# Kernel optimization log

Measured on AMD Instinct MI355X. Metric: run time of the kernel, lower is better.

The kernel has to match this reference:

```python
import jax, jax.numpy as jnp
import numpy as np

# Module hyperparams (from init_kwargs)
VX, VY = 0.16, 0.16
PC_RANGE = (0.0, -39.68, -3.0, 69.12, 39.68, 1.0)
X_OFFSET = VX / 2 + PC_RANGE[0]
Y_OFFSET = VY / 2 + PC_RANGE[1]
X_L = int((PC_RANGE[3] - PC_RANGE[0]) / VX)  # 432
Y_L = int((PC_RANGE[4] - PC_RANGE[1]) / VY)  # 496
IN_CH, OUT_CH = 9, 64
BN_EPS = 1e-3
P, N_MAX, B = 40000, 32, 4


def setup_inputs() -> dict:
    key = jax.random.key(0)
    k1, k2, k3 = jax.random.split(key, 3)
    pillars = jax.random.normal(k1, (P, N_MAX, 4), dtype=jnp.float32)
    # Unique (per batch) pillar coordinates so the scatter is well-defined.
    rng = np.random.default_rng(0)
    per = P // B
    rows = []
    for b in range(B):
        lin = rng.choice(Y_L * X_L, size=per, replace=False)
        ys, xs = lin // X_L, lin % X_L
        rows.append(np.stack([np.full(per, b, np.int32), xs.astype(np.int32), ys.astype(np.int32)], axis=1))
    coors_batch = jnp.asarray(np.concatenate(rows, axis=0))  # (P,3): [b, x, y]
    npoints_per_pillar = jax.random.randint(k2, (P,), 1, N_MAX + 1, dtype=jnp.int32)
    # Learned params: 1x1 Conv1d weight (no bias) + BN affine
    W = jax.random.normal(k3, (OUT_CH, IN_CH), dtype=jnp.float32) * 0.1
    gamma = jnp.ones((OUT_CH,), dtype=jnp.float32)
    beta = jnp.zeros((OUT_CH,), dtype=jnp.float32)
    return {"pillars": pillars, "coors_batch": coors_batch,
            "npoints_per_pillar": npoints_per_pillar,
            "W": W, "gamma": gamma, "beta": beta, "batch_size": B}


def reference(pillars, coors_batch, npoints_per_pillar, W, gamma, beta, batch_size):
    npts = npoints_per_pillar.astype(pillars.dtype)
    # offset of each point from pillar mean (xyz)
    center = jnp.sum(pillars[:, :, :3], axis=1, keepdims=True) / npts[:, None, None]
    offset_pt_center = pillars[:, :, :3] - center                      # (P,N,3)
    cx = coors_batch[:, None, 1:2].astype(pillars.dtype) * VX + X_OFFSET
    cy = coors_batch[:, None, 2:3].astype(pillars.dtype) * VY + Y_OFFSET
    x_off = pillars[:, :, :1] - cx                                     # (P,N,1)
    y_off = pillars[:, :, 1:2] - cy                                    # (P,N,1)
    features = jnp.concatenate([pillars, offset_pt_center, x_off, y_off], axis=-1)  # (P,N,9)
    mask = (jnp.arange(N_MAX)[None, :] < npoints_per_pillar[:, None]).astype(features.dtype)
    features = features * mask[:, :, None]
    # 1x1 Conv1d == per-point channel mix -> (P, C_out, N)
    x = jnp.einsum('pnc,oc->pon', features, W)
    # BatchNorm1d (training-mode stats over pillar and point dims, biased var)
    mean = jnp.mean(x, axis=(0, 2))
    var = jnp.var(x, axis=(0, 2))
    x = gamma[None, :, None] * (x - mean[None, :, None]) * jax.lax.rsqrt(var[None, :, None] + BN_EPS) + beta[None, :, None]
    x = jax.nn.relu(x)
    pooled = jnp.max(x, axis=-1)                                       # (P, C_out)
    # Single vectorized scatter into BEV canvas: (B, Y, X, C) then -> (B, C, Y, X)
    canvas = jnp.zeros((batch_size, Y_L, X_L, OUT_CH), dtype=jnp.float32)
    canvas = canvas.at[coors_batch[:, 0], coors_batch[:, 2], coors_batch[:, 1]].set(pooled)
    return jnp.transpose(canvas, (0, 3, 1, 2))
```

## Files before the change

### kernel.cpp

```cpp
#include <hip/hip_runtime.h>
#include <math.h>

#define P_TOT 40000
#define NMAX 32
#define BATCH 4
#define YL 496
#define XL 432
#define CIN 9
#define COUT 64
#define NTRI 45
#define PN_F 1280000.0f

#define MAP_ELEMS (BATCH * YL * XL)
#define MAP_BYTES (MAP_ELEMS * 4)
#define STATS_OFF MAP_BYTES
#define POOLED_OFF (STATS_OFF + 256)

#define STATS_BLOCKS 512


__global__ __launch_bounds__(256) void k_stats(const float4* __restrict__ pillars,
                                               const int* __restrict__ coors,
                                               const int* __restrict__ npp,
                                               int* __restrict__ map,
                                               float* __restrict__ stats) {
    const int wave = threadIdx.x >> 6;
    const int lane = threadIdx.x & 63;
    const int half = lane >> 5;
    const int n = lane & 31;
    const int gw = blockIdx.x * 4 + wave;
    const int totalWaves = STATS_BLOCKS * 4;

    float s1[CIN];
    float s2[NTRI];
#pragma unroll
    for (int i = 0; i < CIN; i++) s1[i] = 0.0f;
#pragma unroll
    for (int i = 0; i < NTRI; i++) s2[i] = 0.0f;

    for (int p0 = gw * 2; p0 < P_TOT; p0 += totalWaves * 2) {
        int p = p0 + half;
        float4 q = pillars[(size_t)p * NMAX + n];

        float sx = q.x, sy = q.y, sz = q.z;
#pragma unroll
        for (int off = 1; off < 32; off <<= 1) {
            sx += __shfl_xor(sx, off, 32);
            sy += __shfl_xor(sy, off, 32);
            sz += __shfl_xor(sz, off, 32);
        }
        int npts = npp[p];
        float fn = (float)npts;
        float mx = sx / fn, my = sy / fn, mz = sz / fn;

        int xi = coors[p * 3 + 1];
        int yi = coors[p * 3 + 2];
        if (n == 0) {
            int b = coors[p * 3 + 0];
            map[(b * YL + yi) * XL + xi] = p;
        }
        float cx = (float)xi * 0.16f + 0.08f;
        float cy = (float)yi * 0.16f + (-39.6f);

        float msk = (n < npts) ? 1.0f : 0.0f;
        float f[CIN];
        f[0] = q.x * msk; f[1] = q.y * msk; f[2] = q.z * msk; f[3] = q.w * msk;
        f[4] = (q.x - mx) * msk; f[5] = (q.y - my) * msk; f[6] = (q.z - mz) * msk;
        f[7] = (q.x - cx) * msk; f[8] = (q.y - cy) * msk;

        int k = 0;
#pragma unroll
        for (int a = 0; a < CIN; a++) {
            s1[a] += f[a];
#pragma unroll
            for (int c = a; c < CIN; c++) s2[k++] += f[a] * f[c];
        }
    }

#pragma unroll
    for (int i = 0; i < CIN; i++) {
        float v = s1[i];
        for (int off = 1; off < 64; off <<= 1) v += __shfl_xor(v, off, 64);
        s1[i] = v;
    }
#pragma unroll
    for (int i = 0; i < NTRI; i++) {
        float v = s2[i];
        for (int off = 1; off < 64; off <<= 1) v += __shfl_xor(v, off, 64);
        s2[i] = v;
    }

    __shared__ float red[4][54];
    if (lane == 0) {
#pragma unroll
        for (int i = 0; i < CIN; i++) red[wave][i] = s1[i];
#pragma unroll
        for (int i = 0; i < NTRI; i++) red[wave][CIN + i] = s2[i];
    }
    __syncthreads();
    if (threadIdx.x < 54) {
        float v = red[0][threadIdx.x] + red[1][threadIdx.x] +
                  red[2][threadIdx.x] + red[3][threadIdx.x];
        atomicAdd(&stats[threadIdx.x], v);
    }
}

__global__ __launch_bounds__(256) void k_pool(const float4* __restrict__ pillars,
                                              const int* __restrict__ coors,
                                              const int* __restrict__ npp,
                                              const float* __restrict__ W,
                                              float* __restrict__ pooled) {
    int w = threadIdx.x >> 6;
    int lane = threadIdx.x & 63;
    int p = blockIdx.x * 4 + w;
    int n = lane & 31;

    float4 q = pillars[(size_t)p * NMAX + n];
    float sx = q.x, sy = q.y, sz = q.z;
#pragma unroll
    for (int off = 1; off < 32; off <<= 1) {
        sx += __shfl_xor(sx, off, 32);
        sy += __shfl_xor(sy, off, 32);
        sz += __shfl_xor(sz, off, 32);
    }
    int npts = __builtin_amdgcn_readfirstlane(npp[p]);
    float fn = (float)npts;
    float mx = sx / fn, my = sy / fn, mz = sz / fn;
    int xi = coors[p * 3 + 1];
    int yi = coors[p * 3 + 2];
    float cx = (float)xi * 0.16f + 0.08f;
    float cy = (float)yi * 0.16f + (-39.6f);

    const float* wr = W + lane * CIN;
    float w0 = wr[0], w1 = wr[1], w2 = wr[2], w3 = wr[3];
    float w4 = wr[4], w5 = wr[5], w6 = wr[6], w7 = wr[7], w8 = wr[8];
    float A0 = w0 + w4 + w7;
    float A1 = w1 + w5 + w8;
    float A2 = w2 + w6;
    float B = -(w4 * mx + w5 * my + w6 * mz + w7 * cx + w8 * cy);

    float m = (npts < NMAX) ? 0.0f : -INFINITY;
    for (int j = 0; j < npts; ++j) {
        float qx = __uint_as_float(__builtin_amdgcn_readlane(__float_as_uint(q.x), j));
        float qy = __uint_as_float(__builtin_amdgcn_readlane(__float_as_uint(q.y), j));
        float qz = __uint_as_float(__builtin_amdgcn_readlane(__float_as_uint(q.z), j));
        float qw = __uint_as_float(__builtin_amdgcn_readlane(__float_as_uint(q.w), j));
        float d = fmaf(A0, qx, fmaf(A1, qy, fmaf(A2, qz, fmaf(w3, qw, B))));
        m = fmaxf(m, d);
    }
    pooled[(size_t)p * COUT + lane] = m;
}

__global__ __launch_bounds__(256) void k_scatter(const int* __restrict__ map,
                                                 const float* __restrict__ pooled,
                                                 const float* __restrict__ W,
                                                 const float* __restrict__ gamma,
                                                 const float* __restrict__ beta,
                                                 const float* __restrict__ stats,
                                                 float* __restrict__ out) {
    __shared__ float ssc[COUT];
    __shared__ float ssh[COUT];
    if (threadIdx.x < COUT) {
        int o = threadIdx.x;
        float wv[CIN];
#pragma unroll
        for (int c = 0; c < CIN; c++) wv[c] = W[o * CIN + c];

        const float invPN = 1.0f / PN_F;
        float mu = 0.0f;
#pragma unroll
        for (int c = 0; c < CIN; c++) mu += wv[c] * (stats[c] * invPN);

        float ex2 = 0.0f;
        int k = 0;
#pragma unroll
        for (int a = 0; a < CIN; a++) {
#pragma unroll
            for (int c = a; c < CIN; c++) {
                float Mv = stats[CIN + k] * invPN;
                float t = wv[a] * wv[c] * Mv;
                ex2 += (a == c) ? t : 2.0f * t;
                k++;
            }
        }
        float var = ex2 - mu * mu;
        float sc = gamma[o] * rsqrtf(var + 1e-3f);
        ssc[o] = sc;
        ssh[o] = beta[o] - mu * sc;
    }
    __syncthreads();

    int i = blockIdx.x * 256 + threadIdx.x;
    if (i >= BATCH * YL * (XL / 4)) return;
    int x4 = i % (XL / 4);
    int r = i / (XL / 4);
    int y = r % YL;
    int b = r / YL;

    const int4 pid = *(const int4*)(map + (size_t)(b * YL + y) * XL + x4 * 4);
    size_t obase = ((size_t)(b * COUT) * YL + y) * XL + (size_t)x4 * 4;
    const size_t cstride = (size_t)YL * XL;

    const float4 ninf = make_float4(-INFINITY, -INFINITY, -INFINITY, -INFINITY);
#pragma unroll 4
    for (int c4 = 0; c4 < COUT / 4; c4++) {
        float4 r0 = ninf, r1 = ninf, r2 = ninf, r3 = ninf;
        if (pid.x >= 0) r0 = *(const float4*)(pooled + (size_t)pid.x * COUT + c4 * 4);
        if (pid.y >= 0) r1 = *(const float4*)(pooled + (size_t)pid.y * COUT + c4 * 4);
        if (pid.z >= 0) r2 = *(const float4*)(pooled + (size_t)pid.z * COUT + c4 * 4);
        if (pid.w >= 0) r3 = *(const float4*)(pooled + (size_t)pid.w * COUT + c4 * 4);
        float sc0 = ssc[c4 * 4 + 0], sh0 = ssh[c4 * 4 + 0];
        float sc1 = ssc[c4 * 4 + 1], sh1 = ssh[c4 * 4 + 1];
        float sc2 = ssc[c4 * 4 + 2], sh2 = ssh[c4 * 4 + 2];
        float sc3 = ssc[c4 * 4 + 3], sh3 = ssh[c4 * 4 + 3];
        float* o0 = out + obase + (size_t)(c4 * 4) * cstride;
        *(float4*)(o0) = make_float4(
            fmaxf(fmaf(sc0, r0.x, sh0), 0.f), fmaxf(fmaf(sc0, r1.x, sh0), 0.f),
            fmaxf(fmaf(sc0, r2.x, sh0), 0.f), fmaxf(fmaf(sc0, r3.x, sh0), 0.f));
        *(float4*)(o0 + cstride) = make_float4(
            fmaxf(fmaf(sc1, r0.y, sh1), 0.f), fmaxf(fmaf(sc1, r1.y, sh1), 0.f),
            fmaxf(fmaf(sc1, r2.y, sh1), 0.f), fmaxf(fmaf(sc1, r3.y, sh1), 0.f));
        *(float4*)(o0 + 2 * cstride) = make_float4(
            fmaxf(fmaf(sc2, r0.z, sh2), 0.f), fmaxf(fmaf(sc2, r1.z, sh2), 0.f),
            fmaxf(fmaf(sc2, r2.z, sh2), 0.f), fmaxf(fmaf(sc2, r3.z, sh2), 0.f));
        *(float4*)(o0 + 3 * cstride) = make_float4(
            fmaxf(fmaf(sc3, r0.w, sh3), 0.f), fmaxf(fmaf(sc3, r1.w, sh3), 0.f),
            fmaxf(fmaf(sc3, r2.w, sh3), 0.f), fmaxf(fmaf(sc3, r3.w, sh3), 0.f));
    }
}

extern "C" void kernel_launch(void* const* d_in, const int* in_sizes, int n_in,
                              void* d_out, int out_size, void* d_ws, size_t ws_size,
                              hipStream_t stream) {
    const float4* pillars = (const float4*)d_in[0];
    const int* coors = (const int*)d_in[1];
    const int* npp = (const int*)d_in[2];
    const float* W = (const float*)d_in[3];
    const float* gamma = (const float*)d_in[4];
    const float* beta = (const float*)d_in[5];
    float* out = (float*)d_out;

    char* ws = (char*)d_ws;
    int* map = (int*)(ws);
    float* stats = (float*)(ws + STATS_OFF);
    float* pooled = (float*)(ws + POOLED_OFF);

    k_stats<<<STATS_BLOCKS, 256, 0, stream>>>(pillars, coors, npp, map, stats);
    k_pool<<<P_TOT / 4, 256, 0, stream>>>(pillars, coors, npp, W, pooled);
    k_scatter<<<(BATCH * YL * (XL / 4) + 255) / 256, 256, 0, stream>>>(
        map, pooled, W, gamma, beta, stats, out);
}
```

Before: 288.3 us.

## Fuse stats and pooling kernels into a single pass over pillars

Merges the BN-statistics kernel and the pre-BN max-pooling kernel into one grid-stride kernel, so each pillar's points are loaded from global memory once instead of twice and one launch is removed. Each wave now handles two pillars per iteration, using readlane to broadcast per-pillar means and centers, then runs two serial max loops. The cost is a longer dependent chain per iteration with fewer total waves (512 blocks), which may lower latency hiding compared with the previous one-pillar-per-wave pooling grid.

```diff
diff --git a/kernel.cpp b/kernel.cpp
--- a/kernel.cpp
+++ b/kernel.cpp
@@ -16,20 +16,29 @@
 #define STATS_OFF MAP_BYTES
 #define POOLED_OFF (STATS_OFF + 256)
 
-#define STATS_BLOCKS 512
-
-
-__global__ __launch_bounds__(256) void k_stats(const float4* __restrict__ pillars,
-                                               const int* __restrict__ coors,
-                                               const int* __restrict__ npp,
-                                               int* __restrict__ map,
-                                               float* __restrict__ stats) {
+#define SP_BLOCKS 512
+
+
+__global__ __launch_bounds__(256) void k_statspool(const float4* __restrict__ pillars,
+                                                   const int* __restrict__ coors,
+                                                   const int* __restrict__ npp,
+                                                   const float* __restrict__ W,
+                                                   int* __restrict__ map,
+                                                   float* __restrict__ stats,
+                                                   float* __restrict__ pooled) {
     const int wave = threadIdx.x >> 6;
     const int lane = threadIdx.x & 63;
     const int half = lane >> 5;
     const int n = lane & 31;
     const int gw = blockIdx.x * 4 + wave;
-    const int totalWaves = STATS_BLOCKS * 4;
+    const int totalWaves = SP_BLOCKS * 4;
+
+    const float* wr = W + lane * CIN;
+    const float w0 = wr[0], w1 = wr[1], w2 = wr[2], w3 = wr[3];
+    const float w4 = wr[4], w5 = wr[5], w6 = wr[6], w7 = wr[7], w8 = wr[8];
+    const float A0 = w0 + w4 + w7;
+    const float A1 = w1 + w5 + w8;
+    const float A2 = w2 + w6;
 
     float s1[CIN];
     float s2[NTRI];
@@ -75,6 +84,43 @@
 #pragma unroll
             for (int c = a; c < CIN; c++) s2[k++] += f[a] * f[c];
         }
+
+        float mxA = __uint_as_float(__builtin_amdgcn_readlane(__float_as_uint(mx), 0));
+        float myA = __uint_as_float(__builtin_amdgcn_readlane(__float_as_uint(my), 0));
+        float mzA = __uint_as_float(__builtin_amdgcn_readlane(__float_as_uint(mz), 0));
+        float cxA = __uint_as_float(__builtin_amdgcn_readlane(__float_as_uint(cx), 0));
+        float cyA = __uint_as_float(__builtin_amdgcn_readlane(__float_as_uint(cy), 0));
+        int nA = __builtin_amdgcn_readlane(npts, 0);
+        float mxB = __uint_as_float(__builtin_amdgcn_readlane(__float_as_uint(mx), 32));
+        float myB = __uint_as_float(__builtin_amdgcn_readlane(__float_as_uint(my), 32));
+        float mzB = __uint_as_float(__builtin_amdgcn_readlane(__float_as_uint(mz), 32));
+        float cxB = __uint_as_float(__builtin_amdgcn_readlane(__float_as_uint(cx), 32));
+        float cyB = __uint_as_float(__builtin_amdgcn_readlane(__float_as_uint(cy), 32));
+        int nB = __builtin_amdgcn_readlane(npts, 32);
+
+        float BA = -(w4 * mxA + w5 * myA + w6 * mzA + w7 * cxA + w8 * cyA);
+        float BB = -(w4 * mxB + w5 * myB + w6 * mzB + w7 * cxB + w8 * cyB);
+
+        float mA = (nA < NMAX) ? 0.0f : -INFINITY;
+        for (int j = 0; j < nA; ++j) {
+            float qx = __uint_as_float(__builtin_amdgcn_readlane(__float_as_uint(q.x), j));
+            float qy = __uint_as_float(__builtin_amdgcn_readlane(__float_as_uint(q.y), j));
+            float qz = __uint_as_float(__builtin_amdgcn_readlane(__float_as_uint(q.z), j));
+            float qw = __uint_as_float(__builtin_amdgcn_readlane(__float_as_uint(q.w), j));
+            float d = fmaf(A0, qx, fmaf(A1, qy, fmaf(A2, qz, fmaf(w3, qw, BA))));
+            mA = fmaxf(mA, d);
+        }
+        float mB = (nB < NMAX) ? 0.0f : -INFINITY;
+        for (int j = 0; j < nB; ++j) {
+            float qx = __uint_as_float(__builtin_amdgcn_readlane(__float_as_uint(q.x), 32 + j));
+            float qy = __uint_as_float(__builtin_amdgcn_readlane(__float_as_uint(q.y), 32 + j));
+            float qz = __uint_as_float(__builtin_amdgcn_readlane(__float_as_uint(q.z), 32 + j));
+            float qw = __uint_as_float(__builtin_amdgcn_readlane(__float_as_uint(q.w), 32 + j));
+            float d = fmaf(A0, qx, fmaf(A1, qy, fmaf(A2, qz, fmaf(w3, qw, BB))));
+            mB = fmaxf(mB, d);
+        }
+        pooled[(size_t)p0 * COUT + lane] = mA;
+        pooled[(size_t)(p0 + 1) * COUT + lane] = mB;
     }
 
 #pragma unroll
@@ -103,52 +149,6 @@
                   red[2][threadIdx.x] + red[3][threadIdx.x];
         atomicAdd(&stats[threadIdx.x], v);
     }
-}
-
-__global__ __launch_bounds__(256) void k_pool(const float4* __restrict__ pillars,
-                                              const int* __restrict__ coors,
-                                              const int* __restrict__ npp,
-                                              const float* __restrict__ W,
-                                              float* __restrict__ pooled) {
-    int w = threadIdx.x >> 6;
-    int lane = threadIdx.x & 63;
-    int p = blockIdx.x * 4 + w;
-    int n = lane & 31;
-
-    float4 q = pillars[(size_t)p * NMAX + n];
-    float sx = q.x, sy = q.y, sz = q.z;
-#pragma unroll
-    for (int off = 1; off < 32; off <<= 1) {
-        sx += __shfl_xor(sx, off, 32);
-        sy += __shfl_xor(sy, off, 32);
-        sz += __shfl_xor(sz, off, 32);
-    }
-    int npts = __builtin_amdgcn_readfirstlane(npp[p]);
-    float fn = (float)npts;
-    float mx = sx / fn, my = sy / fn, mz = sz / fn;
-    int xi = coors[p * 3 + 1];
-    int yi = coors[p * 3 + 2];
-    float cx = (float)xi * 0.16f + 0.08f;
-    float cy = (float)yi * 0.16f + (-39.6f);
-
-    const float* wr = W + lane * CIN;
-    float w0 = wr[0], w1 = wr[1], w2 = wr[2], w3 = wr[3];
-    float w4 = wr[4], w5 = wr[5], w6 = wr[6], w7 = wr[7], w8 = wr[8];
-    float A0 = w0 + w4 + w7;
-    float A1 = w1 + w5 + w8;
-    float A2 = w2 + w6;
-    float B = -(w4 * mx + w5 * my + w6 * mz + w7 * cx + w8 * cy);
-
-    float m = (npts < NMAX) ? 0.0f : -INFINITY;
-    for (int j = 0; j < npts; ++j) {
-        float qx = __uint_as_float(__builtin_amdgcn_readlane(__float_as_uint(q.x), j));
-        float qy = __uint_as_float(__builtin_amdgcn_readlane(__float_as_uint(q.y), j));
-        float qz = __uint_as_float(__builtin_amdgcn_readlane(__float_as_uint(q.z), j));
-        float qw = __uint_as_float(__builtin_amdgcn_readlane(__float_as_uint(q.w), j));
-        float d = fmaf(A0, qx, fmaf(A1, qy, fmaf(A2, qz, fmaf(w3, qw, B))));
-        m = fmaxf(m, d);
-    }
-    pooled[(size_t)p * COUT + lane] = m;
 }
 
 __global__ __launch_bounds__(256) void k_scatter(const int* __restrict__ map,
@@ -245,8 +245,7 @@
     float* stats = (float*)(ws + STATS_OFF);
     float* pooled = (float*)(ws + POOLED_OFF);
 
-    k_stats<<<STATS_BLOCKS, 256, 0, stream>>>(pillars, coors, npp, map, stats);
-    k_pool<<<P_TOT / 4, 256, 0, stream>>>(pillars, coors, npp, W, pooled);
+    k_statspool<<<SP_BLOCKS, 256, 0, stream>>>(pillars, coors, npp, W, map, stats, pooled);
     k_scatter<<<(BATCH * YL * (XL / 4) + 255) / 256, 256, 0, stream>>>(
         map, pooled, W, gamma, beta, stats, out);
 }
```

Result: faster. 278.2 us, median of 2 (-3.5%).
